# Kernel optimization log

Measured on AMD Instinct MI355X. Metric: run time of the kernel, lower is better.

The kernel has to match this reference:

```python
import jax, jax.numpy as jnp
import numpy as np
from jax import lax

VOCAB, EMBED, HID, B, T = 100, 50, 30, 512, 512
PAD_ID = 0


def setup_inputs() -> dict:
    key = jax.random.key(0)
    ks = jax.random.split(key, 16)
    s_e = 1.0 / np.sqrt(HID)  # torch LSTM/Linear uniform(-1/sqrt(H), 1/sqrt(H)) style
    def u(k, shape, s):
        return jax.random.uniform(k, shape, jnp.float32, -s, s)
    batch_x = jax.random.randint(ks[0], (B, T), 0, VOCAB)
    lens = jax.random.randint(ks[1], (B,), 1, T + 1)
    lens = lens.at[0].set(T)  # ensure pad_packed max length == T
    embedding = jax.random.normal(ks[2], (VOCAB, EMBED), jnp.float32)
    embedding = embedding.at[PAD_ID].set(0.0)  # padding_idx row
    return {
        "batch_x": batch_x,
        "batch_x_lens": lens,
        "embedding": embedding,
        "w_ih1": u(ks[3], (4 * HID, EMBED), s_e),
        "w_hh1": u(ks[4], (4 * HID, HID), s_e),
        "b_ih1": u(ks[5], (4 * HID,), s_e),
        "b_hh1": u(ks[6], (4 * HID,), s_e),
        "w_ih2": u(ks[7], (4 * HID, HID), s_e),
        "w_hh2": u(ks[8], (4 * HID, HID), s_e),
        "b_ih2": u(ks[9], (4 * HID,), s_e),
        "b_hh2": u(ks[10], (4 * HID,), s_e),
        "lw1": u(ks[11], (HID, HID), s_e),
        "lb1": u(ks[12], (HID,), s_e),
        "lw2": u(ks[13], (VOCAB, HID), s_e),
        "lb2": u(ks[14], (VOCAB,), s_e),
    }


def _lstm(x_tbe, mask_tb, w_ih, w_hh, b_ih, b_hh):
    """Masked LSTM over time; state frozen where mask==0 (packed-sequence semantics).
    x_tbe: [T,B,E]; mask_tb: [T,B] bool. Returns hidden seq [T,B,H]."""
    H = w_hh.shape[1]
    Bn = x_tbe.shape[1]
    # precompute input projections for all timesteps (one big GEMM)
    xp = jnp.einsum("tbe,ge->tbg", x_tbe, w_ih) + b_ih + b_hh  # [T,B,4H]

    def step(carry, inp):
        h, c = carry
        xt, mt = inp
        gates = xt + h @ w_hh.T
        i, f, g, o = jnp.split(gates, 4, axis=-1)  # torch gate order i,f,g,o
        i = jax.nn.sigmoid(i)
        f = jax.nn.sigmoid(f)
        g = jnp.tanh(g)
        o = jax.nn.sigmoid(o)
        c_new = f * c + i * g
        h_new = o * jnp.tanh(c_new)
        m = mt[:, None]
        h = jnp.where(m, h_new, h)
        c = jnp.where(m, c_new, c)
        return (h, c), h

    init = (jnp.zeros((Bn, H), x_tbe.dtype), jnp.zeros((Bn, H), x_tbe.dtype))
    _, hs = lax.scan(step, init, (xp, mask_tb))
    return hs


def reference(batch_x, batch_x_lens, embedding,
              w_ih1, w_hh1, b_ih1, b_hh1,
              w_ih2, w_hh2, b_ih2, b_hh2,
              lw1, lb1, lw2, lb2):
    Bn, Tn = batch_x.shape
    mask = (jnp.arange(Tn)[None, :] < batch_x_lens[:, None])  # [B,T]
    x = embedding[batch_x]                                     # [B,T,E]
    x = jnp.transpose(x, (1, 0, 2))                            # [T,B,E]
    m_tb = mask.T                                              # [T,B]
    h1 = _lstm(x, m_tb, w_ih1, w_hh1, b_ih1, b_hh1)            # [T,B,H]
    h2 = _lstm(h1, m_tb, w_ih2, w_hh2, b_ih2, b_hh2)           # [T,B,H]
    out = jnp.transpose(h2, (1, 0, 2))                         # [B,T,H]
    out = jnp.where(mask[:, :, None], out, 0.0)                # pad_packed zero-fill
    hmid = jax.nn.relu(out @ lw1.T + lb1)
    return hmid @ lw2.T + lb2                                  # [B,T,vocab]
```

## Files before the change

kernel.cpp:

```cpp
#include <hip/hip_runtime.h>
#include <math.h>

#define VOCABN 100
#define EMBEDN 50
#define HID 30
#define NB 512
#define NT 512
#define G4 120
#define S 8
#define RD 16

__device__ __forceinline__ float fastrcp(float x) {
  float r;
  asm("v_rcp_f32 %0, %1" : "=v"(r) : "v"(x));
  return r;
}
__device__ __forceinline__ float tanh_fast(float x) {
  return 1.0f - 2.0f * fastrcp(1.0f + __expf(2.0f * x));
}
__device__ __forceinline__ void bcast_halves(float x, float& lo_all, float& hi_all) {
  auto r = __builtin_amdgcn_permlane32_swap(__builtin_bit_cast(unsigned, x),
                                            __builtin_bit_cast(unsigned, x), false, false);
  lo_all = __builtin_bit_cast(float, (unsigned)r[0]);
  hi_all = __builtin_bit_cast(float, (unsigned)r[1]);
}
__device__ __forceinline__ float rdlane(float v, int k) {
  return __builtin_bit_cast(float, __builtin_amdgcn_readlane(__builtin_bit_cast(int, v), k));
}
__device__ __forceinline__ void tick_barrier() {
  asm volatile("s_waitcnt lgkmcnt(0)" ::: "memory");
  __builtin_amdgcn_s_barrier();
  asm volatile("" ::: "memory");
}

__global__ void prep_kernel(const float* __restrict__ emb,
                            const float* __restrict__ w_ih1,
                            const float* __restrict__ b_ih1,
                            const float* __restrict__ b_hh1,
                            const float* __restrict__ b_ih2,
                            const float* __restrict__ b_hh2,
                            const float* __restrict__ lw2,
                            const float* __restrict__ lb1,
                            const float* __restrict__ lb2,
                            float* __restrict__ xpe, float* __restrict__ b2s,
                            float* __restrict__ outc) {
  __shared__ float e[EMBEDN];
  int r = blockIdx.x;
  int tid = threadIdx.x;
  if (tid < EMBEDN) e[tid] = emb[r * EMBEDN + tid];
  __syncthreads();
  if (tid < G4) {
    float s = b_ih1[tid] + b_hh1[tid];
#pragma unroll
    for (int k = 0; k < EMBEDN; ++k) s = fmaf(e[k], w_ih1[tid * EMBEDN + k], s);
    xpe[r * G4 + tid] = s;
    if (r == 0) b2s[tid] = b_ih2[tid] + b_hh2[tid];
  }
  if (r == 0 && tid < VOCABN) {
    float o = lb2[tid];
#pragma unroll
    for (int k = 0; k < HID; ++k) o = fmaf(fmaxf(lb1[k], 0.f), lw2[tid * HID + k], o);
    outc[tid] = o;
  }
}

__global__ void __launch_bounds__(256) scan_kernel(
    const int* __restrict__ batch_x, const int* __restrict__ lens,
    const float* __restrict__ xpe, const float* __restrict__ b2s,
    const float* __restrict__ w_hh1, const float* __restrict__ w_ih2,
    const float* __restrict__ w_hh2,
    const float* __restrict__ lw1, const float* __restrict__ lb1,
    const float* __restrict__ lw2, const float* __restrict__ lb2,
    const float* __restrict__ outc, float* __restrict__ out) {
  __shared__ __align__(16) float h1ring[RD][32];
  __shared__ __align__(16) float2 uring[RD][64];
  __shared__ __align__(16) float h2ring[RD][32];
  __shared__ int tok_lds[NT];

  const int b = blockIdx.x;
  const int tid = threadIdx.x;
  const int wid = tid >> 6;
  const int lane = tid & 63;
  const int half = lane >> 5;
  const int j = lane & 31;
  const int jj = (j < HID) ? j : (HID - 1);
  const int gA = half ? (jj + 2 * HID) : jj;
  const int gB = gA + HID;
  const float bg = half ? 2.0f : 1.0f;

  const int* xrow = batch_x + b * NT;
  for (int i = tid; i < NT; i += 256) tok_lds[i] = xrow[i];

  const int len = lens[b];
  const int K = (len + S - 1) / S;
  __syncthreads();

  if (wid < 3) {
    const float* wsrc = (wid == 0) ? w_hh1 : (wid == 1) ? w_ih2 : w_hh2;
    float wA[HID], wB[HID];
#pragma unroll
    for (int k = 0; k < HID; ++k) {
      wA[k] = wsrc[gA * HID + k];
      wB[k] = wsrc[gB * HID + k];
    }
    const float b2A = b2s[gA], b2B = b2s[gB];

    if (wid == 0) {
      float c1 = 0.f;
      float hs1[HID];
#pragma unroll
      for (int k = 0; k < HID; ++k) hs1[k] = 0.f;
      int tk = tok_lds[0];
      float xa0 = xpe[tk * G4 + gA], xb0 = xpe[tk * G4 + gB];
      tk = tok_lds[1];
      float xa1 = xpe[tk * G4 + gA], xb1 = xpe[tk * G4 + gB];
      tk = tok_lds[2];
      float xa2 = xpe[tk * G4 + gA], xb2 = xpe[tk * G4 + gB];
      int t = 0;
      for (int k = 0; k < K + 3; ++k) {
        if (k < K) {
          int tend = (k + 1) * S;
          tend = (tend < len) ? tend : len;
          for (; t < tend; ++t) {
            float a0a = 0.f, a0b = 0.f, a1a = 0.f, a1b = 0.f;
#pragma unroll
            for (int p = 0; p < 15; ++p) {
              a0a = fmaf(hs1[p], wA[p], a0a);
              a1a = fmaf(hs1[p], wB[p], a1a);
              a0b = fmaf(hs1[p + 15], wA[p + 15], a0b);
              a1b = fmaf(hs1[p + 15], wB[p + 15], a1b);
            }
            float a0 = a0a + a0b + xa0;
            float a1 = a1a + a1b + xb0;
            float sA = 1.0f - bg * fastrcp(1.0f + __expf(bg * a0));
            float sB = 1.0f - fastrcp(1.0f + __expf(a1));
            float i1, g1, f1, o1;
            bcast_halves(sA, i1, g1);
            bcast_halves(sB, f1, o1);
            c1 = fmaf(f1, c1, i1 * g1);
            float h1n = o1 * tanh_fast(c1);
            if (lane < 32) h1ring[t & (RD - 1)][j] = h1n;
#pragma unroll
            for (int q = 0; q < HID; ++q) hs1[q] = rdlane(h1n, q);
            xa0 = xa1; xb0 = xb1;
            xa1 = xa2; xb1 = xb2;
            int tn = t + 3;
            tk = tok_lds[(tn < NT) ? tn : (NT - 1)];
            xa2 = xpe[tk * G4 + gA];
            xb2 = xpe[tk * G4 + gB];
          }
        }
        tick_barrier();
      }
    } else if (wid == 1) {
      int t = 0;
      for (int k = 0; k < K + 3; ++k) {
        if (k >= 1 && k <= K) {
          int tend = k * S;
          tend = (tend < len) ? tend : len;
          for (; t < tend; ++t) {
            const float2* hp = (const float2*)h1ring[t & (RD - 1)];
            float2 hv[15];
#pragma unroll
            for (int p = 0; p < 15; ++p) hv[p] = hp[p];
            float q0a = 0.f, q0b = 0.f, q1a = 0.f, q1b = 0.f;
#pragma unroll
            for (int p = 0; p < 15; ++p) {
              if (p < 8) {
                q0a = fmaf(hv[p].x, wA[2 * p], q0a);
                q1a = fmaf(hv[p].x, wB[2 * p], q1a);
                q0a = fmaf(hv[p].y, wA[2 * p + 1], q0a);
                q1a = fmaf(hv[p].y, wB[2 * p + 1], q1a);
              } else {
                q0b = fmaf(hv[p].x, wA[2 * p], q0b);
                q1b = fmaf(hv[p].x, wB[2 * p], q1b);
                q0b = fmaf(hv[p].y, wA[2 * p + 1], q0b);
                q1b = fmaf(hv[p].y, wB[2 * p + 1], q1b);
              }
            }
            float2 u;
            u.x = q0a + q0b;
            u.y = q1a + q1b;
            uring[t & (RD - 1)][lane] = u;
          }
        }
        tick_barrier();
      }
    } else {
      float c2 = 0.f;
      float hs2[HID];
#pragma unroll
      for (int k = 0; k < HID; ++k) hs2[k] = 0.f;
      int t = 0;
      for (int k = 0; k < K + 3; ++k) {
        if (k >= 2) {
          int tend = (k - 1) * S;
          tend = (tend < len) ? tend : len;
          for (; t < tend; ++t) {
            float2 u = uring[t & (RD - 1)][lane];
            float q0a = 0.f, q0b = 0.f, q1a = 0.f, q1b = 0.f;
#pragma unroll
            for (int p = 0; p < 15; ++p) {
              q0a = fmaf(hs2[p], wA[p], q0a);
              q1a = fmaf(hs2[p], wB[p], q1a);
              q0b = fmaf(hs2[p + 15], wA[p + 15], q0b);
              q1b = fmaf(hs2[p + 15], wB[p + 15], q1b);
            }
            float q0 = q0a + q0b + u.x + b2A;
            float q1 = q1a + q1b + u.y + b2B;
            float uA = 1.0f - bg * fastrcp(1.0f + __expf(bg * q0));
            float uB = 1.0f - fastrcp(1.0f + __expf(q1));
            float i2, g2, f2, o2;
            bcast_halves(uA, i2, g2);
            bcast_halves(uB, f2, o2);
            c2 = fmaf(f2, c2, i2 * g2);
            float h2n = o2 * tanh_fast(c2);
            if (lane < 32) h2ring[t & (RD - 1)][j] = h2n;
#pragma unroll
            for (int q = 0; q < HID; ++q) hs2[q] = rdlane(h2n, q);
          }
        }
        tick_barrier();
      }
    }
  } else {
    const int l1 = (lane < 50) ? lane : 49;
    float w1x[15], w1y[15];
#pragma unroll
    for (int p = 0; p < 15; ++p) {
      w1x[p] = lw1[jj * HID + 2 * p];
      w1y[p] = lw1[jj * HID + 2 * p + 1];
    }
    float w2a[HID], w2b[HID];
#pragma unroll
    for (int k = 0; k < HID; ++k) {
      w2a[k] = lw2[l1 * HID + k];
      w2b[k] = lw2[(l1 + 50) * HID + k];
    }
    const float lb1v = lb1[jj];
    const float lb2a = lb2[l1], lb2b = lb2[l1 + 50];
    const float oca = outc[l1], ocb = outc[l1 + 50];

    int t = 0;
    for (int k = 0; k < K + 3; ++k) {
      if (k >= 3) {
        int tend = (k - 2) * S;
        tend = (tend < len) ? tend : len;
        for (; t < tend; ++t) {
          const float2* hp = (const float2*)h2ring[t & (RD - 1)];
          float2 h[15];
#pragma unroll
          for (int p = 0; p < 15; ++p) h[p] = hp[p];
          float ma = lb1v, mb = 0.f;
#pragma unroll
          for (int p = 0; p < 15; ++p) {
            if (p < 8) {
              ma = fmaf(h[p].x, w1x[p], ma);
              ma = fmaf(h[p].y, w1y[p], ma);
            } else {
              mb = fmaf(h[p].x, w1x[p], mb);
              mb = fmaf(h[p].y, w1y[p], mb);
            }
          }
          float m = fmaxf(ma + mb, 0.f);
          float sm[HID];
#pragma unroll
          for (int q = 0; q < HID; ++q) sm[q] = rdlane(m, q);
          float oa0 = lb2a, oa1 = 0.f, ob0 = lb2b, ob1 = 0.f;
#pragma unroll
          for (int q = 0; q < 15; ++q) {
            oa0 = fmaf(sm[q], w2a[q], oa0);
            ob0 = fmaf(sm[q], w2b[q], ob0);
            oa1 = fmaf(sm[q + 15], w2a[q + 15], oa1);
            ob1 = fmaf(sm[q + 15], w2b[q + 15], ob1);
          }
          float* orow = out + ((size_t)(b * NT + t)) * VOCABN;
          if (lane < 50) {
            orow[l1] = oa0 + oa1;
            orow[l1 + 50] = ob0 + ob1;
          }
        }
      }
      tick_barrier();
    }
    for (int tt = len; tt < NT; ++tt) {
      float* orow = out + ((size_t)(b * NT + tt)) * VOCABN;
      if (lane < 50) {
        orow[l1] = oca;
        orow[l1 + 50] = ocb;
      }
    }
  }
}

extern "C" void kernel_launch(void* const* d_in, const int* in_sizes, int n_in,
                              void* d_out, int out_size, void* d_ws, size_t ws_size,
                              hipStream_t stream) {
  const int* batch_x = (const int*)d_in[0];
  const int* lens = (const int*)d_in[1];
  const float* emb = (const float*)d_in[2];
  const float* w_ih1 = (const float*)d_in[3];
  const float* w_hh1 = (const float*)d_in[4];
  const float* b_ih1 = (const float*)d_in[5];
  const float* b_hh1 = (const float*)d_in[6];
  const float* w_ih2 = (const float*)d_in[7];
  const float* w_hh2 = (const float*)d_in[8];
  const float* b_ih2 = (const float*)d_in[9];
  const float* b_hh2 = (const float*)d_in[10];
  const float* lw1 = (const float*)d_in[11];
  const float* lb1 = (const float*)d_in[12];
  const float* lw2 = (const float*)d_in[13];
  const float* lb2 = (const float*)d_in[14];
  float* out = (float*)d_out;

  char* ws = (char*)d_ws;
  float* xpe = (float*)ws;
  float* b2s = (float*)(ws + 48 * 1024);
  float* outc = (float*)(ws + 56 * 1024);

  prep_kernel<<<VOCABN, 128, 0, stream>>>(emb, w_ih1, b_ih1, b_hh1, b_ih2, b_hh2,
                                          lw2, lb1, lb2, xpe, b2s, outc);
  scan_kernel<<<NB, 256, 0, stream>>>(batch_x, lens, xpe, b2s, w_hh1, w_ih2, w_hh2,
                                      lw1, lb1, lw2, lb2, outc, out);
}
```

Measured before the change: 266.8 us.

## Fold log2(e) scaling into weights and use raw exp2; double sync interval

Pre-scales the input projections, biases and recurrent weights by log2(e) (2*log2(e) for the tanh gate) so the gate activations call v_exp_f32 directly, with no multiply inside __expf. The cell state is kept pre-scaled through the i gate so the final tanh needs no extra multiply either. This shortens the serial dependency chain of each recurrent step. Separately, the barrier interval between pipeline stages doubles and the ring buffer depth grows to match, halving the number of block barriers but adding pipeline fill latency.

```diff
diff --git a/kernel.cpp b/kernel.cpp
--- a/kernel.cpp
+++ b/kernel.cpp
@@ -7,16 +7,21 @@
 #define NB 512
 #define NT 512
 #define G4 120
-#define S 8
-#define RD 16
+#define S 16
+#define RD 32
+
+#define L2E 1.44269504089f
+#define L2E2 2.88539008178f
 
 __device__ __forceinline__ float fastrcp(float x) {
   float r;
   asm("v_rcp_f32 %0, %1" : "=v"(r) : "v"(x));
   return r;
 }
-__device__ __forceinline__ float tanh_fast(float x) {
-  return 1.0f - 2.0f * fastrcp(1.0f + __expf(2.0f * x));
+__device__ __forceinline__ float fexp2(float x) {
+  float r;
+  asm("v_exp_f32 %0, %1" : "=v"(r) : "v"(x));
+  return r;
 }
 __device__ __forceinline__ void bcast_halves(float x, float& lo_all, float& hi_all) {
   auto r = __builtin_amdgcn_permlane32_swap(__builtin_bit_cast(unsigned, x),
@@ -53,8 +58,9 @@
     float s = b_ih1[tid] + b_hh1[tid];
 #pragma unroll
     for (int k = 0; k < EMBEDN; ++k) s = fmaf(e[k], w_ih1[tid * EMBEDN + k], s);
-    xpe[r * G4 + tid] = s;
-    if (r == 0) b2s[tid] = b_ih2[tid] + b_hh2[tid];
+    float sc = (tid >= 2 * HID && tid < 3 * HID) ? L2E2 : L2E;
+    xpe[r * G4 + tid] = s * sc;
+    if (r == 0) b2s[tid] = (b_ih2[tid] + b_hh2[tid]) * sc;
   }
   if (r == 0 && tid < VOCABN) {
     float o = lb2[tid];
@@ -86,7 +92,6 @@
   const int jj = (j < HID) ? j : (HID - 1);
   const int gA = half ? (jj + 2 * HID) : jj;
   const int gB = gA + HID;
-  const float bg = half ? 2.0f : 1.0f;
 
   const int* xrow = batch_x + b * NT;
   for (int i = tid; i < NT; i += 256) tok_lds[i] = xrow[i];
@@ -96,17 +101,20 @@
   __syncthreads();
 
   if (wid < 3) {
+    const float C1 = half ? 1.0f : L2E2;
+    const float C2 = half ? 2.0f : L2E2;
+    const float scA = half ? L2E2 : L2E;
     const float* wsrc = (wid == 0) ? w_hh1 : (wid == 1) ? w_ih2 : w_hh2;
     float wA[HID], wB[HID];
 #pragma unroll
     for (int k = 0; k < HID; ++k) {
-      wA[k] = wsrc[gA * HID + k];
-      wB[k] = wsrc[gB * HID + k];
+      wA[k] = wsrc[gA * HID + k] * scA;
+      wB[k] = wsrc[gB * HID + k] * L2E;
     }
     const float b2A = b2s[gA], b2B = b2s[gB];
 
     if (wid == 0) {
-      float c1 = 0.f;
+      float cs1 = 0.f;
       float hs1[HID];
 #pragma unroll
       for (int k = 0; k < HID; ++k) hs1[k] = 0.f;
@@ -132,13 +140,14 @@
             }
             float a0 = a0a + a0b + xa0;
             float a1 = a1a + a1b + xb0;
-            float sA = 1.0f - bg * fastrcp(1.0f + __expf(bg * a0));
-            float sB = 1.0f - fastrcp(1.0f + __expf(a1));
-            float i1, g1, f1, o1;
-            bcast_halves(sA, i1, g1);
+            float sA = C1 - C2 * fastrcp(1.0f + fexp2(a0));
+            float sB = 1.0f - fastrcp(1.0f + fexp2(a1));
+            float iL, g1, f1, o1;
+            bcast_halves(sA, iL, g1);
             bcast_halves(sB, f1, o1);
-            c1 = fmaf(f1, c1, i1 * g1);
-            float h1n = o1 * tanh_fast(c1);
+            cs1 = fmaf(f1, cs1, iL * g1);
+            float rr = fastrcp(1.0f + fexp2(cs1));
+            float h1n = fmaf(-2.0f * o1, rr, o1);
             if (lane < 32) h1ring[t & (RD - 1)][j] = h1n;
 #pragma unroll
             for (int q = 0; q < HID; ++q) hs1[q] = rdlane(h1n, q);
@@ -187,7 +196,7 @@
         tick_barrier();
       }
     } else {
-      float c2 = 0.f;
+      float cs2 = 0.f;
       float hs2[HID];
 #pragma unroll
       for (int k = 0; k < HID; ++k) hs2[k] = 0.f;
@@ -208,13 +217,14 @@
             }
             float q0 = q0a + q0b + u.x + b2A;
             float q1 = q1a + q1b + u.y + b2B;
-            float uA = 1.0f - bg * fastrcp(1.0f + __expf(bg * q0));
-            float uB = 1.0f - fastrcp(1.0f + __expf(q1));
-            float i2, g2, f2, o2;
-            bcast_halves(uA, i2, g2);
-            bcast_halves(uB, f2, o2);
-            c2 = fmaf(f2, c2, i2 * g2);
-            float h2n = o2 * tanh_fast(c2);
+            float sA = C1 - C2 * fastrcp(1.0f + fexp2(q0));
+            float sB = 1.0f - fastrcp(1.0f + fexp2(q1));
+            float iL, g2, f2, o2;
+            bcast_halves(sA, iL, g2);
+            bcast_halves(sB, f2, o2);
+            cs2 = fmaf(f2, cs2, iL * g2);
+            float rr = fastrcp(1.0f + fexp2(cs2));
+            float h2n = fmaf(-2.0f * o2, rr, o2);
             if (lane < 32) h2ring[t & (RD - 1)][j] = h2n;
 #pragma unroll
             for (int q = 0; q < HID; ++q) hs2[q] = rdlane(h2n, q);
```

Measured after the change: 268.9 us. No clear change (+0.8%).
